# Optimization experiments

Measured on AMD Instinct MI355X. Metric: run time of the kernel, lower is better.

Reference implementation:

```python
import jax, jax.numpy as jnp
import numpy as np

B, S, E, H = 2, 2048, 1024, 16
D = E // H  # head_dim = 64

def setup_inputs() -> dict:
    key = jax.random.key(0)
    ks = jax.random.split(key, 5)
    scale = 0.02
    return {
        "x": jax.random.normal(ks[0], (B, S, E), dtype=jnp.float32),
        "Wq": jax.random.normal(ks[1], (E, E), dtype=jnp.float32) * scale,
        "Wk": jax.random.normal(ks[2], (E, E), dtype=jnp.float32) * scale,
        "Wv": jax.random.normal(ks[3], (E, E), dtype=jnp.float32) * scale,
        "Wo": jax.random.normal(ks[4], (E, E), dtype=jnp.float32) * scale,
        "bo": jnp.zeros((E,), dtype=jnp.float32),
    }

def reference(x, Wq, Wk, Wv, Wo, bo):
    b, s, e = x.shape
    # Linear projections (torch Linear: x @ W.T), split heads -> (b, h, s, d)
    q = (x @ Wq.T).reshape(b, s, H, D).transpose(0, 2, 1, 3)
    k = (x @ Wk.T).reshape(b, s, H, D).transpose(0, 2, 1, 3)
    v = (x @ Wv.T).reshape(b, s, H, D).transpose(0, 2, 1, 3)
    # Full materialized causal scores (b, h, s, s)
    scores = jnp.einsum("bhqd,bhkd->bhqk", q, k)
    causal = jnp.tril(jnp.ones((s, s), dtype=bool))  # True = keep
    scores = jnp.where(causal, scores, -jnp.inf)
    attn = jax.nn.softmax(scores / jnp.sqrt(jnp.float32(D)), axis=-1)
    ctx = jnp.einsum("bhqk,bhkd->bhqd", attn, v)
    ctx = ctx.transpose(0, 2, 1, 3).reshape(b, s, e)
    return ctx @ Wo.T + bo
```

## Files before the change

kernel.cpp:

```cpp
#include <hip/hip_runtime.h>
#include <hip/hip_bf16.h>

typedef __attribute__((ext_vector_type(8))) short short8_t;
typedef __attribute__((ext_vector_type(4))) short s4v;
typedef __attribute__((ext_vector_type(4))) float f32x4_t;
using u16 = unsigned short;

constexpr int S_LEN = 2048;
constexpr int EMB   = 1024;
constexpr int NH    = 16;
constexpr int HD    = 64;
constexpr int BATCH = 2;
constexpr int MR    = BATCH * S_LEN;
constexpr int E3    = 3 * EMB;

#define L2E 1.44269504f

__device__ __forceinline__ u16 f2bf(float f) {
  unsigned u = __builtin_bit_cast(unsigned, f);
  unsigned r = 0x7fffu + ((u >> 16) & 1u);
  return (u16)((u + r) >> 16);
}

__device__ __forceinline__ void gld16(const void* g, void* l) {
  __builtin_amdgcn_global_load_lds(
      (const __attribute__((address_space(1))) void*)g,
      (__attribute__((address_space(3))) void*)l, 16, 0, 0);
}

template <int OFF>
__device__ __forceinline__ s4v tr16(const __attribute__((address_space(3))) u16* p) {
  s4v d;
  asm volatile("ds_read_b64_tr_b16 %0, %1 offset:%2"
               : "=v"(d) : "v"(p), "n"(OFF));
  return d;
}

__global__ void k_cvt_all(const float* __restrict__ x, const float* __restrict__ Wq,
                          const float* __restrict__ Wk, const float* __restrict__ Wv,
                          const float* __restrict__ Wo, u16* __restrict__ out) {
  int i = blockIdx.x * 256 + threadIdx.x;
  const float* src;
  int j;
  float sc = 1.0f;
  if (i < (1 << 20)) {
    src = x; j = i;
  } else {
    int jj = i - (1 << 20);
    int r = jj >> 18;
    j = jj & ((1 << 18) - 1);
    src = (r == 0) ? Wq : (r == 1) ? Wk : (r == 2) ? Wv : Wo;
    if (r == 0) sc = 0.125f;
  }
  float4 v = reinterpret_cast<const float4*>(src)[j];
  ushort4 o;
  o.x = f2bf(v.x * sc); o.y = f2bf(v.y * sc);
  o.z = f2bf(v.z * sc); o.w = f2bf(v.w * sc);
  reinterpret_cast<ushort4*>(out)[i] = o;
}

template <bool F32OUT>
__global__ __launch_bounds__(256) void k_gemm_bt(
    const u16* __restrict__ A, const u16* __restrict__ Bw,
    void* __restrict__ Cv, const float* __restrict__ bias,
    int M, int N, int K) {
  __shared__ short As[128 * 32];
  __shared__ short Bs[128 * 32];
  const int t    = threadIdx.x;
  const int w    = t >> 6;
  const int ln15 = t & 15;
  const int lg   = (t >> 4) & 3;
  const int wr   = w >> 1, wc = w & 1;
  const int m0   = blockIdx.y * 128, n0 = blockIdx.x * 128;

  const int srow = t >> 2;
  const int scol = (t & 3) * 8;
  const u16* gA = A + (size_t)(m0 + srow) * K + scol;
  const u16* gB = Bw + (size_t)(n0 + srow) * K + scol;
  short* lA = As + w * 512;
  short* lB = Bs + w * 512;

  f32x4_t acc[4][4] = {};

  for (int k0 = 0; k0 < K; k0 += 32) {
    gld16(gA + k0, lA);
    gld16(gA + (size_t)64 * K + k0, lA + 2048);
    gld16(gB + k0, lB);
    gld16(gB + (size_t)64 * K + k0, lB + 2048);
    __syncthreads();
    short8_t af[4], bf[4];
#pragma unroll
    for (int i = 0; i < 4; ++i) {
      af[i] = *reinterpret_cast<const short8_t*>(
          &As[(wr * 64 + i * 16 + ln15) * 32 + 8 * lg]);
      bf[i] = *reinterpret_cast<const short8_t*>(
          &Bs[(wc * 64 + i * 16 + ln15) * 32 + 8 * lg]);
    }
#pragma unroll
    for (int i = 0; i < 4; ++i)
#pragma unroll
      for (int j = 0; j < 4; ++j)
        acc[i][j] = __builtin_amdgcn_mfma_f32_16x16x32_bf16(
            af[i], bf[j], acc[i][j], 0, 0, 0);
    __syncthreads();
  }

  if (F32OUT) {
    float* C = reinterpret_cast<float*>(Cv);
#pragma unroll
    for (int i = 0; i < 4; ++i)
#pragma unroll
      for (int j = 0; j < 4; ++j) {
        const int col = n0 + wc * 64 + j * 16 + ln15;
        const float bv = bias ? bias[col] : 0.0f;
#pragma unroll
        for (int r = 0; r < 4; ++r) {
          const int row = m0 + wr * 64 + i * 16 + lg * 4 + r;
          C[(size_t)row * N + col] = acc[i][j][r] + bv;
        }
      }
  } else {
    u16* C = reinterpret_cast<u16*>(Cv);
#pragma unroll
    for (int i = 0; i < 4; ++i)
#pragma unroll
      for (int j = 0; j < 4; ++j) {
        const int col = n0 + wc * 64 + j * 16 + ln15;
#pragma unroll
        for (int r = 0; r < 4; ++r) {
          const int row = m0 + wr * 64 + i * 16 + lg * 4 + r;
          C[(size_t)row * N + col] = f2bf(acc[i][j][r]);
        }
      }
  }
}

__global__ __launch_bounds__(256, 4) void k_attn2(const u16* __restrict__ QKV,
                                                  u16* __restrict__ ctx) {
  __shared__ u16 Ks[2][64 * 64];
  __shared__ u16 Vs[2][64 * 64];

  const int t    = threadIdx.x;
  const int w    = t >> 6;
  const int l    = t & 63;
  const int ln15 = t & 15;
  const int lg   = (l >> 4) & 3;

  const int by = blockIdx.y;
  const int r8 = by & 7, k4 = by >> 3;
  const int qt = (k4 == 0) ? (31 - r8) : (k4 == 1) ? (15 - r8)
               : (k4 == 2) ? r8 : (16 + r8);
  const int bh = blockIdx.x;
  const int b  = bh >> 4, h = bh & 15;

  const u16* KVb = QKV + (size_t)b * S_LEN * E3 + h * HD;
  const u16* Kg  = KVb + 1024;
  const u16* Vg  = KVb + 2048;
  const int qrow = qt * 64 + w * 16;

  short8_t qf[2];
  {
    const u16* qp = KVb + (size_t)(qrow + ln15) * E3 + 8 * lg;
    qf[0] = *reinterpret_cast<const short8_t*>(qp);
    qf[1] = *reinterpret_cast<const short8_t*>(qp + 32);
  }

  const int krow_lo = l >> 3;
  const int kcol    = 8 * ((l & 7) ^ krow_lo);
  const int vkv     = l >> 1;
  const int vcol    = 16 * w + 8 * (l & 1);

  const int kx  = 8 * (ln15 & 7);
  const int kc0 = (8 * lg) ^ kx;
  const int kc1 = (32 + 8 * lg) ^ kx;

#define STAGE(buf, kv0)                                                        \
  do {                                                                         \
    gld16(Kg + (size_t)((kv0) + 16 * w + krow_lo) * E3 + kcol,                 \
          &Ks[buf][1024 * w]);                                                 \
    gld16(Kg + (size_t)((kv0) + 16 * w + 8 + krow_lo) * E3 + kcol,             \
          &Ks[buf][1024 * w + 512]);                                           \
    gld16(Vg + (size_t)((kv0) + vkv) * E3 + vcol, &Vs[buf][1024 * w]);         \
    gld16(Vg + (size_t)((kv0) + 32 + vkv) * E3 + vcol,                         \
          &Vs[buf][1024 * w + 512]);                                           \
  } while (0)

  f32x4_t o[4] = {};
  float mrow = -3e38f, lrow = 0.0f;
  const int nt_tiles = qt + 1;

  STAGE(0, 0);
  int cur = 0;

  for (int kvt = 0; kvt < nt_tiles; ++kvt) {
    const int kv0 = kvt * 64;
    asm volatile("s_barrier" ::: "memory");
    if (kvt + 1 < nt_tiles) {
      STAGE(cur ^ 1, kv0 + 64);
      asm volatile("s_waitcnt vmcnt(4)" ::: "memory");
    } else {
      asm volatile("s_waitcnt vmcnt(0)" ::: "memory");
    }
    asm volatile("s_barrier" ::: "memory");

    const __attribute__((address_space(3))) u16* vp =
        (const __attribute__((address_space(3))) u16*)&Vs[cur][4 * l];
    s4v vf[4][2][2];
#pragma unroll
    for (int nt = 0; nt < 4; ++nt) {
      if (nt == 0) { vf[0][0][0]=tr16<0>(vp);    vf[0][0][1]=tr16<512>(vp);
                     vf[0][1][0]=tr16<1024>(vp); vf[0][1][1]=tr16<1536>(vp); }
      if (nt == 1) { vf[1][0][0]=tr16<2048>(vp); vf[1][0][1]=tr16<2560>(vp);
                     vf[1][1][0]=tr16<3072>(vp); vf[1][1][1]=tr16<3584>(vp); }
      if (nt == 2) { vf[2][0][0]=tr16<4096>(vp); vf[2][0][1]=tr16<4608>(vp);
                     vf[2][1][0]=tr16<5120>(vp); vf[2][1][1]=tr16<5632>(vp); }
      if (nt == 3) { vf[3][0][0]=tr16<6144>(vp); vf[3][0][1]=tr16<6656>(vp);
                     vf[3][1][0]=tr16<7168>(vp); vf[3][1][1]=tr16<7680>(vp); }
    }

    f32x4_t tacc[4];
#pragma unroll
    for (int ks = 0; ks < 4; ++ks) {
      const int R = 16 * ks + ln15;
      short8_t kf0 = *reinterpret_cast<const short8_t*>(&Ks[cur][R * 64 + kc0]);
      short8_t kf1 = *reinterpret_cast<const short8_t*>(&Ks[cur][R * 64 + kc1]);
      f32x4_t a = {0.f, 0.f, 0.f, 0.f};
      a = __builtin_amdgcn_mfma_f32_16x16x32_bf16(kf0, qf[0], a, 0, 0, 0);
      a = __builtin_amdgcn_mfma_f32_16x16x32_bf16(kf1, qf[1], a, 0, 0, 0);
      tacc[ks] = a;
    }

    if (kvt == qt) {
      const int qg = qrow + ln15;
#pragma unroll
      for (int ks = 0; ks < 4; ++ks)
#pragma unroll
        for (int r = 0; r < 4; ++r)
          if (kv0 + 16 * ks + 4 * lg + r > qg) tacc[ks][r] = -3e38f;
    }

    float rm = -3e38f;
#pragma unroll
    for (int ks = 0; ks < 4; ++ks)
#pragma unroll
      for (int r = 0; r < 4; ++r) rm = fmaxf(rm, tacc[ks][r]);
    rm = fmaxf(rm, __shfl_xor(rm, 16, 64));
    rm = fmaxf(rm, __shfl_xor(rm, 32, 64));
    const float nm = fmaxf(mrow, rm);
    const float sc_old = exp2f((mrow - nm) * L2E);
    mrow = nm;

    float p[4][4];
    float rs = 0.0f;
#pragma unroll
    for (int ks = 0; ks < 4; ++ks)
#pragma unroll
      for (int r = 0; r < 4; ++r) {
        const float pv = exp2f((tacc[ks][r] - nm) * L2E);
        p[ks][r] = pv;
        rs += pv;
      }
    rs += __shfl_xor(rs, 16, 64);
    rs += __shfl_xor(rs, 32, 64);
    lrow = lrow * sc_old + rs;

#pragma unroll
    for (int r = 0; r < 4; ++r) {
      const float so = __shfl(sc_old, 20 * lg + r, 64);
#pragma unroll
      for (int nt = 0; nt < 4; ++nt) o[nt][r] *= so;
    }

    short8_t pf[2];
#pragma unroll
    for (int s2 = 0; s2 < 2; ++s2)
#pragma unroll
      for (int j = 0; j < 4; ++j) {
        pf[s2][j]     = (short)f2bf(p[2 * s2][j]);
        pf[s2][j + 4] = (short)f2bf(p[2 * s2 + 1][j]);
      }

    asm volatile("s_waitcnt lgkmcnt(0)");
    __builtin_amdgcn_sched_barrier(0);

#pragma unroll
    for (int nt = 0; nt < 4; ++nt) {
#pragma unroll
      for (int s2 = 0; s2 < 2; ++s2) {
        short8_t bv = __builtin_shufflevector(vf[nt][s2][0], vf[nt][s2][1],
                                              0, 1, 2, 3, 4, 5, 6, 7);
        o[nt] = __builtin_amdgcn_mfma_f32_16x16x32_bf16(pf[s2], bv, o[nt], 0, 0, 0);
      }
    }
    cur ^= 1;
  }
#undef STAGE

  const float linv = 1.0f / lrow;
#pragma unroll
  for (int r = 0; r < 4; ++r) {
    const float li = __shfl(linv, 20 * lg + r, 64);
    u16* op = ctx + (size_t)(b * S_LEN + qrow + 4 * lg + r) * EMB + h * HD;
#pragma unroll
    for (int nt = 0; nt < 4; ++nt)
      op[nt * 16 + ln15] = f2bf(o[nt][r] * li);
  }
}

extern "C" void kernel_launch(void* const* d_in, const int* in_sizes, int n_in,
                              void* d_out, int out_size, void* d_ws, size_t ws_size,
                              hipStream_t stream) {
  const float* x  = (const float*)d_in[0];
  const float* Wq = (const float*)d_in[1];
  const float* Wk = (const float*)d_in[2];
  const float* Wv = (const float*)d_in[3];
  const float* Wo = (const float*)d_in[4];
  const float* bo = (const float*)d_in[5];

  u16* ws   = (u16*)d_ws;
  u16* xb   = ws;
  u16* wcat = xb + (size_t)MR * EMB;
  u16* wob  = wcat + (size_t)3 * EMB * EMB;
  u16* qkv  = wob + (size_t)EMB * EMB;
  u16* ctxb = qkv + (size_t)MR * E3;

  k_cvt_all<<<8192, 256, 0, stream>>>(x, Wq, Wk, Wv, Wo, xb);

  k_gemm_bt<false><<<dim3(E3 / 128, MR / 128), 256, 0, stream>>>(
      xb, wcat, qkv, nullptr, MR, E3, EMB);

  k_attn2<<<dim3(BATCH * NH, 32), 256, 0, stream>>>(qkv, ctxb);

  k_gemm_bt<true><<<dim3(EMB / 128, MR / 128), 256, 0, stream>>>(
      ctxb, wob, d_out, bo, MR, EMB, EMB);
}
```

Baseline: 127.9 us.

## Skip softmax rescale when max unchanged, add MFMA priority, simplify tile order

Adds a wave-uniform check so the output and row-sum rescale by the old max runs only when some row's max increased. The exponent becomes a single fma. Tree-shaped max reductions replace the serial chain, and s_setprio raises wave priority around the QK and PV MFMA blocks. The interleaved query-tile mapping is replaced by a plain heaviest-first order, which changes load balancing across CUs.

```diff
diff --git a/kernel.cpp b/kernel.cpp
--- a/kernel.cpp
+++ b/kernel.cpp
@@ -146,10 +146,7 @@
   const int ln15 = t & 15;
   const int lg   = (l >> 4) & 3;
 
-  const int by = blockIdx.y;
-  const int r8 = by & 7, k4 = by >> 3;
-  const int qt = (k4 == 0) ? (31 - r8) : (k4 == 1) ? (15 - r8)
-               : (k4 == 2) ? r8 : (16 + r8);
+  const int qt = 31 - blockIdx.y;
   const int bh = blockIdx.x;
   const int b  = bh >> 4, h = bh & 15;
 
@@ -219,6 +216,7 @@
     }
 
     f32x4_t tacc[4];
+    __builtin_amdgcn_s_setprio(1);
 #pragma unroll
     for (int ks = 0; ks < 4; ++ks) {
       const int R = 16 * ks + ln15;
@@ -229,6 +227,7 @@
       a = __builtin_amdgcn_mfma_f32_16x16x32_bf16(kf1, qf[1], a, 0, 0, 0);
       tacc[ks] = a;
     }
+    __builtin_amdgcn_s_setprio(0);
 
     if (kvt == qt) {
       const int qg = qrow + ln15;
@@ -239,37 +238,41 @@
           if (kv0 + 16 * ks + 4 * lg + r > qg) tacc[ks][r] = -3e38f;
     }
 
-    float rm = -3e38f;
-#pragma unroll
-    for (int ks = 0; ks < 4; ++ks)
-#pragma unroll
-      for (int r = 0; r < 4; ++r) rm = fmaxf(rm, tacc[ks][r]);
+    float rm = fmaxf(
+        fmaxf(fmaxf(fmaxf(tacc[0][0], tacc[0][1]), fmaxf(tacc[0][2], tacc[0][3])),
+              fmaxf(fmaxf(tacc[1][0], tacc[1][1]), fmaxf(tacc[1][2], tacc[1][3]))),
+        fmaxf(fmaxf(fmaxf(tacc[2][0], tacc[2][1]), fmaxf(tacc[2][2], tacc[2][3])),
+              fmaxf(fmaxf(tacc[3][0], tacc[3][1]), fmaxf(tacc[3][2], tacc[3][3]))));
     rm = fmaxf(rm, __shfl_xor(rm, 16, 64));
     rm = fmaxf(rm, __shfl_xor(rm, 32, 64));
-    const float nm = fmaxf(mrow, rm);
-    const float sc_old = exp2f((mrow - nm) * L2E);
-    mrow = nm;
-
+
+    if (__any(rm > mrow)) {
+      const float nm = fmaxf(mrow, rm);
+      const float sc = exp2f((mrow - nm) * L2E);
+      mrow = nm;
+      lrow *= sc;
+#pragma unroll
+      for (int r = 0; r < 4; ++r) {
+        const float so = __shfl(sc, 20 * lg + r, 64);
+#pragma unroll
+        for (int nt = 0; nt < 4; ++nt) o[nt][r] *= so;
+      }
+    }
+
+    const float nmL = mrow * L2E;
     float p[4][4];
     float rs = 0.0f;
 #pragma unroll
     for (int ks = 0; ks < 4; ++ks)
 #pragma unroll
       for (int r = 0; r < 4; ++r) {
-        const float pv = exp2f((tacc[ks][r] - nm) * L2E);
+        const float pv = exp2f(fmaf(tacc[ks][r], L2E, -nmL));
         p[ks][r] = pv;
         rs += pv;
       }
     rs += __shfl_xor(rs, 16, 64);
     rs += __shfl_xor(rs, 32, 64);
-    lrow = lrow * sc_old + rs;
-
-#pragma unroll
-    for (int r = 0; r < 4; ++r) {
-      const float so = __shfl(sc_old, 20 * lg + r, 64);
-#pragma unroll
-      for (int nt = 0; nt < 4; ++nt) o[nt][r] *= so;
-    }
+    lrow += rs;
 
     short8_t pf[2];
 #pragma unroll
@@ -283,6 +286,7 @@
     asm volatile("s_waitcnt lgkmcnt(0)");
     __builtin_amdgcn_sched_barrier(0);
 
+    __builtin_amdgcn_s_setprio(1);
 #pragma unroll
     for (int nt = 0; nt < 4; ++nt) {
 #pragma unroll
@@ -292,6 +296,7 @@
         o[nt] = __builtin_amdgcn_mfma_f32_16x16x32_bf16(pf[s2], bv, o[nt], 0, 0, 0);
       }
     }
+    __builtin_amdgcn_s_setprio(0);
     cur ^= 1;
   }
 #undef STAGE
```

Measured after the change: 127.8 us. Within noise of the previous version (-0.1%).
